# Optimization experiments

Measured on AMD Instinct MI355X. Metric: run time of the kernel, lower is better.

The kernel has to match this reference:

```python
import jax, jax.numpy as jnp
import numpy as np
from jax import lax


def setup_inputs() -> dict:
    key = jax.random.key(0)
    k1, k2 = jax.random.split(key)
    B, T, C, U, W = 8, 4096, 512, 512, 2
    inputs = jax.random.normal(k1, (B, T, C), dtype=jnp.float32)
    kernel = jax.random.normal(k2, (W, C, 3 * U), dtype=jnp.float32) * (1.0 / np.sqrt(W * C))
    bias = jnp.zeros((3 * U,), dtype=jnp.float32)
    return {"inputs": inputs, "kernel": kernel, "bias": bias}


def _fo_pool(x, f):
    # x, f: [B, T, U]; c_t = f_t * c_{t-1} + (1 - f_t) * x_t, c_0 = 0
    xT = jnp.swapaxes(x, 0, 1)  # [T, B, U]
    fT = jnp.swapaxes(f, 0, 1)
    c0 = jnp.zeros(x.shape[:1] + x.shape[2:], dtype=x.dtype)  # [B, U]

    def step(c, fx):
        ft, xt = fx
        c = ft * c + (1.0 - ft) * xt
        return c, c

    _, cT = lax.scan(step, c0, (fT, xT))
    return jnp.swapaxes(cT, 0, 1)  # [B, T, U]


def reference(inputs, kernel, bias):
    # Conv1D, padding='same', stride=1, NWC layout
    gates = lax.conv_general_dilated(
        inputs, kernel, window_strides=(1,), padding='SAME',
        dimension_numbers=('NWC', 'WIO', 'NWC')) + bias  # [B, T, 3U]
    x, forget, output = jnp.split(gates, 3, axis=-1)
    x = jnp.tanh(x)
    forget = jax.nn.sigmoid(forget)
    c = _fo_pool(x, forget)
    h = jax.nn.sigmoid(output) * c
    return h
```

## Files before the change

kernel.cpp:

```cpp
#include <hip/hip_runtime.h>

typedef unsigned short u16;
typedef unsigned int u32;
typedef _Float16 f16;
typedef __attribute__((ext_vector_type(8))) _Float16 half8;
typedef __attribute__((ext_vector_type(2))) __fp16 fp16x2;
typedef __attribute__((ext_vector_type(4))) float float4_;
typedef __attribute__((ext_vector_type(4))) unsigned short ushort4_;
typedef __attribute__((ext_vector_type(4))) unsigned int u32x4;

union hu { f16 h; u16 u; };

__device__ __forceinline__ u32 pkrtz(float a, float b) {
    fp16x2 t = __builtin_amdgcn_cvt_pkrtz(a, b);
    union { fp16x2 h; u32 u; } cv; cv.h = t;
    return cv.u;
}

__device__ __forceinline__ void gl16(const u16* g, u16* l) {
    __builtin_amdgcn_global_load_lds(
        (const __attribute__((address_space(1))) void*)g,
        (__attribute__((address_space(3))) void*)l, 16, 0, 0);
}

#define Bsz 8
#define Tsz 4096
#define Csz 512
#define Usz 512
#define NG  1536
#define KK  1024
#define MM  32768
#define NCH 128
#define CHL 32

__global__ void prep_a(const float* __restrict__ in, u16* __restrict__ A16) {
    int gid = blockIdx.x * 256 + threadIdx.x;
    int idx8 = gid * 8;
    int c8 = idx8 & 511;
    int row = idx8 >> 9;
    int b = (u32)row / 4097u;
    int t = row - b * 4097;
    u32x4 w;
    if (t == Tsz) {
        w = (u32x4)0;
    } else {
        const float* p = in + ((size_t)(b * Tsz + t) << 9) + c8;
        float4_ v0 = *(const float4_*)p;
        float4_ v1 = *(const float4_*)(p + 4);
        w.x = pkrtz(v0.x, v0.y); w.y = pkrtz(v0.z, v0.w);
        w.z = pkrtz(v1.x, v1.y); w.w = pkrtz(v1.z, v1.w);
    }
    *(u32x4*)(A16 + idx8) = w;
}

__global__ void prep_k(const float* __restrict__ kern, u16* __restrict__ KT) {
    __shared__ u16 t[64][70];
    const int k0 = blockIdx.x * 64;
    const int n0 = blockIdx.y * 64;
    const int tid = threadIdx.x;
    #pragma unroll
    for (int it = 0; it < 16; ++it) {
        int s = it * 256 + tid;
        int r = s >> 6;
        int c = s & 63;
        float v = kern[(size_t)(k0 + r) * NG + n0 + c];
        hu cv; cv.h = (f16)v;
        t[c][r] = cv.u;
    }
    __syncthreads();
    #pragma unroll
    for (int it = 0; it < 4; ++it) {
        int s = it * 256 + tid;
        int n = s >> 4;
        int kq = (s & 15) * 4;
        ushort4_ w;
        w.x = t[n][kq]; w.y = t[n][kq + 1]; w.z = t[n][kq + 2]; w.w = t[n][kq + 3];
        *(ushort4_*)(KT + (size_t)(n0 + n) * KK + k0 + kq) = w;
    }
}

__global__ __launch_bounds__(256, 4) void gemm_gates(
    const u16* __restrict__ A16, const u16* __restrict__ KT,
    const float* __restrict__ bias,
    u16* __restrict__ X, u16* __restrict__ F, float* __restrict__ O)
{
    __shared__ u16 lA[8192], lB[8192];

    const int tid  = threadIdx.x;
    const int lane = tid & 63;
    const int wave = tid >> 6;

    const int orig = blockIdx.x;
    const int wg = (orig & 7) * 384 + (orig >> 3);
    const int nb = wg % 12;
    const int mb = wg / 12;
    const int m0 = mb * 128;
    const int n0 = nb * 128;
    const int b  = m0 >> 12;
    const int t0 = m0 & 4095;
    const int arow0 = b * (Tsz + 1) + t0;

    float4_ acc[4][4];
    #pragma unroll
    for (int i = 0; i < 4; ++i)
        #pragma unroll
        for (int j = 0; j < 4; ++j) acc[i][j] = (float4_)0.0f;

    const int wm = (wave >> 1) * 64;
    const int wn = (wave & 1) * 64;
    const int ar = wm + (lane & 15);
    const int br = wn + (lane & 15);
    const int q  = lane >> 4;
    const int swz = lane & 7;

    for (int kc = 0; kc < KK; kc += 64) {
        __syncthreads();
        const int tap = kc >> 9;
        const int kin = kc & 511;
        const int ab = arow0 + tap;
        #pragma unroll
        for (int it = 0; it < 4; ++it) {
            const int s = it * 256 + tid;
            const int row = s >> 3, p = s & 7;
            const int c = p ^ (row & 7);
            gl16(A16 + (((size_t)(ab + row)) << 9) + kin + c * 8, lA + (s - lane) * 8);
        }
        #pragma unroll
        for (int it = 0; it < 4; ++it) {
            const int s = it * 256 + tid;
            const int row = s >> 3, p = s & 7;
            const int c = p ^ (row & 7);
            gl16(KT + (((size_t)(n0 + row)) << 10) + kc + c * 8, lB + (s - lane) * 8);
        }
        __syncthreads();

        #pragma unroll
        for (int s2 = 0; s2 < 2; ++s2) {
            half8 fa[4], fb[4];
            const int cc = (s2 * 4 + q) ^ swz;
            #pragma unroll
            for (int i = 0; i < 4; ++i) {
                fa[i] = *(const half8*)(lA + (ar + i * 16) * 64 + cc * 8);
                fb[i] = *(const half8*)(lB + (br + i * 16) * 64 + cc * 8);
            }
            #pragma unroll
            for (int mi = 0; mi < 4; ++mi)
                #pragma unroll
                for (int ni = 0; ni < 4; ++ni)
                    acc[mi][ni] = __builtin_amdgcn_mfma_f32_16x16x32_f16(fa[mi], fb[ni], acc[mi][ni], 0, 0, 0);
        }
    }

    const int plane = nb >> 2;
    const int rq = q * 4;
    const int cl = lane & 15;
    #pragma unroll
    for (int mi = 0; mi < 4; ++mi)
        #pragma unroll
        for (int ni = 0; ni < 4; ++ni) {
            const int gm = m0 + wm + mi * 16 + rq;
            const int gn = n0 + wn + ni * 16 + cl;
            const float bv = bias[gn];
            const int cp = gn & 511;
            #pragma unroll
            for (int r2 = 0; r2 < 4; ++r2) {
                float v = acc[mi][ni][r2] + bv;
                if (plane == 0) {
                    float res = 1.0f - 2.0f / (__expf(2.0f * v) + 1.0f);
                    hu cv; cv.h = (f16)res;
                    X[(size_t)(gm + r2) * Usz + cp] = cv.u;
                } else if (plane == 1) {
                    float res = 1.0f / (1.0f + __expf(-v));
                    hu cv; cv.h = (f16)res;
                    F[(size_t)(gm + r2) * Usz + cp] = cv.u;
                } else {
                    float res = 1.0f / (1.0f + __expf(-v));
                    O[(size_t)(gm + r2) * Usz + cp] = res;
                }
            }
        }
}

__device__ __forceinline__ float4_ x4(const u16* p) {
    ushort4_ xr = *(const ushort4_*)p;
    float4_ xv;
    #pragma unroll
    for (int j = 0; j < 4; ++j) { hu cv; cv.u = xr[j]; xv[j] = (float)cv.h; }
    return xv;
}

__global__ void scan_chunk(const u16* __restrict__ F, const u16* __restrict__ X,
                           float* __restrict__ CA, float* __restrict__ CB) {
    int g = blockIdx.x * 256 + threadIdx.x;
    int u4 = (g & 127) * 4;
    int bc = g >> 7;
    size_t base = (size_t)bc * CHL * Usz + u4;
    float4_ c = (float4_)0.0f, A = (float4_)1.0f;
    for (int i = 0; i < CHL; ++i) {
        float4_ fv = x4(F + base + (size_t)i * Usz);
        float4_ xv = x4(X + base + (size_t)i * Usz);
        c = fv * c + (1.0f - fv) * xv;
        A = A * fv;
    }
    *(float4_*)(CA + (size_t)bc * Usz + u4) = A;
    *(float4_*)(CB + (size_t)bc * Usz + u4) = c;
}

__global__ void scan_prefix(const float* __restrict__ CA, const float* __restrict__ CB,
                            float* __restrict__ CS) {
    int g = blockIdx.x * 256 + threadIdx.x;
    int u = g & 511;
    int b = g >> 9;
    float c = 0.0f;
    #pragma unroll 16
    for (int ch = 0; ch < NCH; ++ch) {
        int idx = (b * NCH + ch) * Usz + u;
        CS[idx] = c;
        c = CA[idx] * c + CB[idx];
    }
}

__global__ void scan_final(const u16* __restrict__ F, const u16* __restrict__ X,
                           const float* __restrict__ CS, float* __restrict__ out) {
    int g = blockIdx.x * 256 + threadIdx.x;
    int u4 = (g & 127) * 4;
    int bc = g >> 7;
    size_t base = (size_t)bc * CHL * Usz + u4;
    float4_ c = *(const float4_*)(CS + (size_t)bc * Usz + u4);
    for (int i = 0; i < CHL; ++i) {
        float4_ fv = x4(F + base + (size_t)i * Usz);
        float4_ xv = x4(X + base + (size_t)i * Usz);
        c = fv * c + (1.0f - fv) * xv;
        float4_ ov = *(const float4_*)(out + base + (size_t)i * Usz);
        *(float4_*)(out + base + (size_t)i * Usz) = ov * c;
    }
}

extern "C" void kernel_launch(void* const* d_in, const int* in_sizes, int n_in,
                              void* d_out, int out_size, void* d_ws, size_t ws_size,
                              hipStream_t stream) {
    const float* in   = (const float*)d_in[0];
    const float* kern = (const float*)d_in[1];
    const float* bias = (const float*)d_in[2];
    float* out = (float*)d_out;
    char* ws = (char*)d_ws;

    const size_t A16_B  = (size_t)Bsz * (Tsz + 1) * Csz * 2;
    const size_t OFF_KT = A16_B;
    const size_t OFF_F  = OFF_KT + (size_t)NG * KK * 2;
    const size_t OFF_X  = OFF_F + (size_t)MM * Usz * 2;
    const size_t NEED   = OFF_X + (size_t)MM * Usz * 2;

    if (ws_size < NEED) return;

    u16*   A16 = (u16*)ws;
    u16*   KT  = (u16*)(ws + OFF_KT);
    u16*   Fh  = (u16*)(ws + OFF_F);
    u16*   Xb  = (u16*)(ws + OFF_X);
    const size_t CH = (size_t)Bsz * NCH * Usz;
    float* CA = (float*)ws;
    float* CB = CA + CH;
    float* CS = CB + CH;

    prep_a<<<(int)(A16_B / 16 / 256), 256, 0, stream>>>(in, A16);
    prep_k<<<dim3(KK / 64, NG / 64), 256, 0, stream>>>(kern, KT);
    gemm_gates<<<(MM / 128) * (NG / 128), 256, 0, stream>>>(A16, KT, bias, Xb, Fh, out);
    scan_chunk<<<Bsz * NCH * Usz / 4 / 256, 256, 0, stream>>>(Fh, Xb, CA, CB);
    scan_prefix<<<Bsz * Usz / 256, 256, 0, stream>>>(CA, CB, CS);
    scan_final<<<Bsz * NCH * Usz / 4 / 256, 256, 0, stream>>>(Fh, Xb, CS, out);
}
```

Measured before the change: 292.6 us.

## Halve scan chunk length, prefetch scan loads, raise GEMM occupancy bound

Doubles the number of scan chunks (each chunk now covers 16 timesteps), so the chunk and final scan kernels launch twice as many threads, each with a shorter serial dependency chain. The per-chunk loops are fully unrolled with explicit one-step-ahead register prefetch of the F/X loads. The GEMM launch bound is raised from 4 to 5 blocks per SM. The risks are a longer serial prefix pass over 256 chunks and register spills in the GEMM under the tighter register budget.

After: 350.4 us. +19.8%, slower.

```diff
diff --git a/kernel.cpp b/kernel.cpp
--- a/kernel.cpp
+++ b/kernel.cpp
@@ -30,8 +30,8 @@
 #define NG  1536
 #define KK  1024
 #define MM  32768
-#define NCH 128
-#define CHL 32
+#define NCH 256
+#define CHL 16
 
 __global__ void prep_a(const float* __restrict__ in, u16* __restrict__ A16) {
     int gid = blockIdx.x * 256 + threadIdx.x;
@@ -79,7 +79,7 @@
     }
 }
 
-__global__ __launch_bounds__(256, 4) void gemm_gates(
+__global__ __launch_bounds__(256, 5) void gemm_gates(
     const u16* __restrict__ A16, const u16* __restrict__ KT,
     const float* __restrict__ bias,
     u16* __restrict__ X, u16* __restrict__ F, float* __restrict__ O)
@@ -189,30 +189,48 @@
     return xv;
 }
 
-__global__ void scan_chunk(const u16* __restrict__ F, const u16* __restrict__ X,
-                           float* __restrict__ CA, float* __restrict__ CB) {
+__device__ __forceinline__ float4_ cvt4(ushort4_ xr) {
+    float4_ xv;
+    #pragma unroll
+    for (int j = 0; j < 4; ++j) { hu cv; cv.u = xr[j]; xv[j] = (float)cv.h; }
+    return xv;
+}
+
+__global__ __launch_bounds__(256) void scan_chunk(
+    const u16* __restrict__ F, const u16* __restrict__ X,
+    float* __restrict__ CA, float* __restrict__ CB) {
     int g = blockIdx.x * 256 + threadIdx.x;
     int u4 = (g & 127) * 4;
     int bc = g >> 7;
     size_t base = (size_t)bc * CHL * Usz + u4;
     float4_ c = (float4_)0.0f, A = (float4_)1.0f;
+    ushort4_ fcur = *(const ushort4_*)(F + base);
+    ushort4_ xcur = *(const ushort4_*)(X + base);
+    #pragma unroll
     for (int i = 0; i < CHL; ++i) {
-        float4_ fv = x4(F + base + (size_t)i * Usz);
-        float4_ xv = x4(X + base + (size_t)i * Usz);
+        ushort4_ fnx = fcur, xnx = xcur;
+        if (i + 1 < CHL) {
+            fnx = *(const ushort4_*)(F + base + (size_t)(i + 1) * Usz);
+            xnx = *(const ushort4_*)(X + base + (size_t)(i + 1) * Usz);
+        }
+        float4_ fv = cvt4(fcur);
+        float4_ xv = cvt4(xcur);
         c = fv * c + (1.0f - fv) * xv;
         A = A * fv;
+        fcur = fnx; xcur = xnx;
     }
     *(float4_*)(CA + (size_t)bc * Usz + u4) = A;
     *(float4_*)(CB + (size_t)bc * Usz + u4) = c;
 }
 
-__global__ void scan_prefix(const float* __restrict__ CA, const float* __restrict__ CB,
-                            float* __restrict__ CS) {
+__global__ __launch_bounds__(256) void scan_prefix(
+    const float* __restrict__ CA, const float* __restrict__ CB,
+    float* __restrict__ CS) {
     int g = blockIdx.x * 256 + threadIdx.x;
     int u = g & 511;
     int b = g >> 9;
     float c = 0.0f;
-    #pragma unroll 16
+    #pragma unroll 8
     for (int ch = 0; ch < NCH; ++ch) {
         int idx = (b * NCH + ch) * Usz + u;
         CS[idx] = c;
@@ -220,19 +238,29 @@
     }
 }
 
-__global__ void scan_final(const u16* __restrict__ F, const u16* __restrict__ X,
-                           const float* __restrict__ CS, float* __restrict__ out) {
+__global__ __launch_bounds__(256) void scan_final(
+    const u16* __restrict__ F, const u16* __restrict__ X,
+    const float* __restrict__ CS, float* __restrict__ out) {
     int g = blockIdx.x * 256 + threadIdx.x;
     int u4 = (g & 127) * 4;
     int bc = g >> 7;
     size_t base = (size_t)bc * CHL * Usz + u4;
     float4_ c = *(const float4_*)(CS + (size_t)bc * Usz + u4);
+    ushort4_ fcur = *(const ushort4_*)(F + base);
+    ushort4_ xcur = *(const ushort4_*)(X + base);
+    #pragma unroll
     for (int i = 0; i < CHL; ++i) {
-        float4_ fv = x4(F + base + (size_t)i * Usz);
-        float4_ xv = x4(X + base + (size_t)i * Usz);
+        ushort4_ fnx = fcur, xnx = xcur;
+        if (i + 1 < CHL) {
+            fnx = *(const ushort4_*)(F + base + (size_t)(i + 1) * Usz);
+            xnx = *(const ushort4_*)(X + base + (size_t)(i + 1) * Usz);
+        }
+        float4_ fv = cvt4(fcur);
+        float4_ xv = cvt4(xcur);
         c = fv * c + (1.0f - fv) * xv;
         float4_ ov = *(const float4_*)(out + base + (size_t)i * Usz);
         *(float4_*)(out + base + (size_t)i * Usz) = ov * c;
+        fcur = fnx; xcur = xnx;
     }
 }
 
```
